# Optimization experiments

Hardware: AMD Instinct MI355X
Metric: run time of the kernel (lower is better)

## Reference

```python
import jax, jax.numpy as jnp
import numpy as np

BATCH = 64
INPUT_LENGTH = 128
N_TERMINALS = 64
N_NONTERMINALS = 128


def setup_inputs() -> dict:
    key = jax.random.key(0)
    k1, k2, k3 = jax.random.split(key, 3)
    input_tensor = jax.random.uniform(k1, (BATCH, INPUT_LENGTH, N_TERMINALS), dtype=jnp.float32)
    terminal_productions = jax.random.normal(k2, (N_NONTERMINALS, N_TERMINALS), dtype=jnp.float32)
    nonterminal_productions = jax.random.normal(k3, (N_NONTERMINALS, N_NONTERMINALS, N_TERMINALS), dtype=jnp.float32)
    return {
        "input_tensor": input_tensor,
        "terminal_productions": terminal_productions,
        "nonterminal_productions": nonterminal_productions,
    }


def reference(input_tensor, terminal_productions, nonterminal_productions):
    # input_tensor: [B, L, T]
    tp = jax.nn.sigmoid(terminal_productions)            # [N, T]
    ntp = jax.nn.sigmoid(nonterminal_productions)        # [N, N, T]

    # step 0: terminal production choices
    tpc = jnp.einsum('nt,bt->bn', tp, input_tensor[:, 0])  # [B, N]
    out0 = tpc[:, 0]                                        # [B]

    def step(carry, x_i):
        prev_choices, prev_out = carry                     # [B, N], [B]
        # per-batch nonterminal production choice matrix: [B, N, N]
        npc = jnp.clip(jnp.einsum('nmt,bt->bnm', ntp, x_i), 0.0, 1.0)
        cur = jnp.clip(jnp.einsum('bnm,bm->bn', npc, prev_choices), 0.0, 1.0)
        mask = x_i[:, N_TERMINALS - 1]                     # [B]
        out = prev_out * mask + cur[:, 0] * (1.0 - mask)
        return (cur, out), None

    xs = jnp.swapaxes(input_tensor[:, 1:], 0, 1)           # [L-1, B, T]
    (final_choices, final_out), _ = jax.lax.scan(step, (tpc, out0), xs)
    return final_out[:, None]                              # [B, 1]
```

## Files before the change

kernel.cpp:

```cpp
#include <hip/hip_runtime.h>
#include <hip/hip_bf16.h>

typedef unsigned int u32;
typedef unsigned char u8;
typedef _Float16 f16;
typedef f16 f16x2 __attribute__((ext_vector_type(2)));
typedef short s16x8 __attribute__((ext_vector_type(8)));
typedef float f32x4 __attribute__((ext_vector_type(4)));

#define BB 64
#define LL 128
#define TT 64
#define NN 128
#define NM (NN*NN)

__device__ __forceinline__ float sigf(float v) {
    return 1.0f / (1.0f + __expf(-v));
}

__device__ __forceinline__ float clip01(float v) {
    return fminf(fmaxf(v, 0.f), 1.f);
}

__device__ __forceinline__ u32 f2bf(float f) {
    u32 u = __builtin_bit_cast(u32, f);
    return (u + 0x7fffu + ((u >> 16) & 1u)) >> 16;
}

__device__ __forceinline__ float fdot2f(f16x2 wa, f16x2 xa, float ca) {
#if defined(__HIP_DEVICE_COMPILE__) && __has_builtin(__builtin_amdgcn_fdot2)
    return __builtin_amdgcn_fdot2(wa, xa, ca, false);
#else
    return ca + (float)wa[0] * (float)xa[0] + (float)wa[1] * (float)xa[1];
#endif
}

__device__ __forceinline__ u32 ud4(u32 a, u32 b, u32 c) {
#if defined(__HIP_DEVICE_COMPILE__) && __has_builtin(__builtin_amdgcn_udot4)
    return __builtin_amdgcn_udot4(a, b, c, false);
#else
    return c + (a & 255u) * (b & 255u) + ((a >> 8) & 255u) * ((b >> 8) & 255u)
             + ((a >> 16) & 255u) * ((b >> 16) & 255u) + (a >> 24) * (b >> 24);
#endif
}

__global__ __launch_bounds__(256) void pack_w(const float* __restrict__ ntp,
                                              ushort* __restrict__ wpk) {
    const int g = blockIdx.x * 256 + threadIdx.x;
    const int l = g & 63, h = (g >> 6) & 1, i = g >> 7;
    const int row = i * 16 + (l & 15);
    const int t0 = h * 32 + ((l >> 4) << 3);
    const float* src = ntp + row * 64 + t0;
    float4 f0 = *reinterpret_cast<const float4*>(src);
    float4 f1 = *reinterpret_cast<const float4*>(src + 4);
    float v[8] = {f0.x, f0.y, f0.z, f0.w, f1.x, f1.y, f1.z, f1.w};
    u32 o[4];
    #pragma unroll
    for (int q = 0; q < 4; ++q)
        o[q] = f2bf(sigf(v[2 * q])) | (f2bf(sigf(v[2 * q + 1])) << 16);
    uint4 ov; ov.x = o[0]; ov.y = o[1]; ov.z = o[2]; ov.w = o[3];
    *reinterpret_cast<uint4*>(wpk + (size_t)g * 8) = ov;
}

__global__ __launch_bounds__(256) void pack_x(const float* __restrict__ x_all,
                                              ushort* __restrict__ xpk) {
    const int g = blockIdx.x * 256 + threadIdx.x;
    const int l = g & 63, h = (g >> 6) & 1, j = (g >> 7) & 7, b = g >> 10;
    const int s = j * 16 + (l & 15);
    const int t0 = h * 32 + ((l >> 4) << 3);
    const float* src = x_all + ((size_t)b * LL + s) * TT + t0;
    float4 f0 = *reinterpret_cast<const float4*>(src);
    float4 f1 = *reinterpret_cast<const float4*>(src + 4);
    float v[8] = {f0.x, f0.y, f0.z, f0.w, f1.x, f1.y, f1.z, f1.w};
    u32 o[4];
    #pragma unroll
    for (int q = 0; q < 4; ++q)
        o[q] = f2bf(v[2 * q]) | (f2bf(v[2 * q + 1]) << 16);
    uint4 ov; ov.x = o[0]; ov.y = o[1]; ov.z = o[2]; ov.w = o[3];
    *reinterpret_cast<uint4*>(xpk + (size_t)g * 8) = ov;
}

__global__ __launch_bounds__(256) void gemm_mfma(const ushort* __restrict__ wpk,
                                                 const ushort* __restrict__ xpk,
                                                 u8* __restrict__ npc) {
    __shared__ __align__(16) u8 stg[4][16384];
    const int b = blockIdx.x >> 4;
    const int nb = blockIdx.x & 15;
    const int wv = threadIdx.x >> 6, l = threadIdx.x & 63;

    uint4 xf[8][2];
    #pragma unroll
    for (int j = 0; j < 8; ++j)
        #pragma unroll
        for (int h = 0; h < 2; ++h)
            xf[j][h] = *reinterpret_cast<const uint4*>(
                xpk + (size_t)(((b * 8 + j) * 2 + h) * 64 + l) * 8);

    const int c = l & 15, r0 = (l >> 4) * 4;
    u8* stw = stg[wv];
    const int khi  = (nb >> 3) * 8;
    const int nlow = (nb & 7) * 8;

    for (int mg2 = 0; mg2 < 2; ++mg2) {
        const int mg = wv * 2 + mg2;
        #pragma unroll
        for (int n_l = 0; n_l < 8; ++n_l) {
            const int i = (nb * 8 + n_l) * 8 + mg;
            uint4 a0 = *reinterpret_cast<const uint4*>(wpk + (size_t)((i * 2 + 0) * 64 + l) * 8);
            uint4 a1 = *reinterpret_cast<const uint4*>(wpk + (size_t)((i * 2 + 1) * 64 + l) * 8);
            const f32x4 z = {0.f, 0.f, 0.f, 0.f};
            f32x4 acc[8];
            #pragma unroll
            for (int j = 0; j < 8; ++j)
                acc[j] = __builtin_amdgcn_mfma_f32_16x16x32_bf16(
                    __builtin_bit_cast(s16x8, a0), __builtin_bit_cast(s16x8, xf[j][0]), z, 0, 0, 0);
            #pragma unroll
            for (int j = 0; j < 8; ++j)
                acc[j] = __builtin_amdgcn_mfma_f32_16x16x32_bf16(
                    __builtin_bit_cast(s16x8, a1), __builtin_bit_cast(s16x8, xf[j][1]), acc[j], 0, 0, 0);

            const int sk = (((n_l + c) & 7) << 4) + r0;
            #pragma unroll
            for (int j = 0; j < 8; ++j) {
                u32 w = 0;
                #pragma unroll
                for (int r = 0; r < 4; ++r) {
                    float q = clip01(acc[j][r]) * 255.f + 0.5f;
                    w |= ((u32)q) << (8 * r);
                }
                *reinterpret_cast<u32*>(stw + j * 2048 + c * 128 + sk) = w;
            }
        }
        asm volatile("s_waitcnt lgkmcnt(0)" ::: "memory");
        __builtin_amdgcn_sched_barrier(0);

        const int nr = l & 7;
        #pragma unroll
        for (int j = 0; j < 8; ++j) {
            #pragma unroll
            for (int half = 0; half < 2; ++half) {
                const int cc = half * 8 + (l >> 3);
                uint4 v = *reinterpret_cast<const uint4*>(
                    stw + j * 2048 + cc * 128 + (((nr + cc) & 7) << 4));
                *reinterpret_cast<uint4*>(npc + ((size_t)b << 21) + ((size_t)j << 18)
                    + ((size_t)cc << 14) + ((size_t)(mg + khi) << 10)
                    + ((nlow + nr) << 4)) = v;
            }
        }
        asm volatile("s_waitcnt lgkmcnt(0)" ::: "memory");
        __builtin_amdgcn_sched_barrier(0);
    }
}

__global__ __launch_bounds__(64) void recur4(const float* __restrict__ x_all,
                                             const float* __restrict__ tp,
                                             const u8* __restrict__ npc,
                                             float* __restrict__ outp) {
    __shared__ __align__(16) u8 prev_lds[2][128];
    __shared__ float masks_lds[128];
    __shared__ float tpc_lds[128];
    __shared__ float x0_lds[64];

    const int b = blockIdx.x, l = threadIdx.x;
    const u8* npcl = npc + ((size_t)b << 21) + ((size_t)l << 4);

    x0_lds[l] = x_all[(size_t)b * 8192 + l];
    masks_lds[l]      = x_all[(size_t)b * 8192 + l * 64 + 63];
    masks_lds[64 + l] = x_all[(size_t)b * 8192 + (64 + l) * 64 + 63];
    asm volatile("s_waitcnt lgkmcnt(0)" ::: "memory");
    __builtin_amdgcn_sched_barrier(0);

#define LOADSET(R, T) do { \
        int _t = (T) <= 127 ? (T) : 127; \
        const u8* _p = npcl + ((size_t)(_t >> 4) << 18) + ((size_t)(_t & 15) << 14); \
        _Pragma("unroll") \
        for (int _k = 0; _k < 16; ++_k) \
            R[_k] = *reinterpret_cast<const uint4*>(_p + _k * 1024); \
    } while (0)

    uint4 nA[16], nB[16];
    LOADSET(nA, 1);

    float a0 = 0.f, a1 = 0.f;
    #pragma unroll
    for (int t4 = 0; t4 < 16; ++t4) {
        float4 xv = *reinterpret_cast<const float4*>(x0_lds + t4 * 4);
        float4 w0 = *reinterpret_cast<const float4*>(tp + l * 64 + t4 * 4);
        float4 w1 = *reinterpret_cast<const float4*>(tp + (64 + l) * 64 + t4 * 4);
        a0 += sigf(w0.x) * xv.x; a0 += sigf(w0.y) * xv.y;
        a0 += sigf(w0.z) * xv.z; a0 += sigf(w0.w) * xv.w;
        a1 += sigf(w1.x) * xv.x; a1 += sigf(w1.y) * xv.y;
        a1 += sigf(w1.z) * xv.z; a1 += sigf(w1.w) * xv.w;
    }
    tpc_lds[l] = a0; tpc_lds[64 + l] = a1;
    float out_r = a0;
    asm volatile("s_waitcnt lgkmcnt(0)" ::: "memory");
    __builtin_amdgcn_sched_barrier(0);

    {
        float s0f = 0.f, s1f = 0.f;
        #pragma unroll
        for (int k = 0; k < 8; ++k) {
            u32 ax[4] = {nA[k].x, nA[k].y, nA[k].z, nA[k].w};
            u32 bx[4] = {nA[k + 8].x, nA[k + 8].y, nA[k + 8].z, nA[k + 8].w};
            #pragma unroll
            for (int w = 0; w < 4; ++w) {
                float4 tv = *reinterpret_cast<const float4*>(tpc_lds + k * 16 + w * 4);
                u32 aw = ax[w], bw = bx[w];
                s0f += (float)(aw & 255u) * tv.x + (float)((aw >> 8) & 255u) * tv.y
                     + (float)((aw >> 16) & 255u) * tv.z + (float)(aw >> 24) * tv.w;
                s1f += (float)(bw & 255u) * tv.x + (float)((bw >> 8) & 255u) * tv.y
                     + (float)((bw >> 16) & 255u) * tv.z + (float)(bw >> 24) * tv.w;
            }
        }
        float c0 = clip01(s0f * (1.f / 255.f));
        float c1 = clip01(s1f * (1.f / 255.f));
        float mk = masks_lds[1];
        if (l == 0) out_r = out_r * mk + c0 * (1.f - mk);
        prev_lds[0][l]      = (u8)(c0 * 255.f + 0.5f);
        prev_lds[0][64 + l] = (u8)(c1 * 255.f + 0.5f);
        asm volatile("s_waitcnt lgkmcnt(0)" ::: "memory");
        __builtin_amdgcn_sched_barrier(0);
    }

    int p = 0;
    LOADSET(nA, 2); LOADSET(nB, 3);

#define STEP(R, S) do { \
        uint4 pv[8]; \
        _Pragma("unroll") \
        for (int _q = 0; _q < 8; ++_q) \
            pv[_q] = *reinterpret_cast<const uint4*>(&prev_lds[p][_q * 16]); \
        float mk = masks_lds[(S)]; \
        u32 s0 = 0, t0 = 0, s1 = 0, t1 = 0; \
        _Pragma("unroll") \
        for (int _k = 0; _k < 4; ++_k) { \
            s0 = ud4(R[_k].x, pv[_k].x, s0); s0 = ud4(R[_k].y, pv[_k].y, s0); \
            s0 = ud4(R[_k].z, pv[_k].z, s0); s0 = ud4(R[_k].w, pv[_k].w, s0); \
        } \
        _Pragma("unroll") \
        for (int _k = 4; _k < 8; ++_k) { \
            t0 = ud4(R[_k].x, pv[_k].x, t0); t0 = ud4(R[_k].y, pv[_k].y, t0); \
            t0 = ud4(R[_k].z, pv[_k].z, t0); t0 = ud4(R[_k].w, pv[_k].w, t0); \
        } \
        _Pragma("unroll") \
        for (int _k = 8; _k < 12; ++_k) { \
            s1 = ud4(R[_k].x, pv[_k - 8].x, s1); s1 = ud4(R[_k].y, pv[_k - 8].y, s1); \
            s1 = ud4(R[_k].z, pv[_k - 8].z, s1); s1 = ud4(R[_k].w, pv[_k - 8].w, s1); \
        } \
        _Pragma("unroll") \
        for (int _k = 12; _k < 16; ++_k) { \
            t1 = ud4(R[_k].x, pv[_k - 8].x, t1); t1 = ud4(R[_k].y, pv[_k - 8].y, t1); \
            t1 = ud4(R[_k].z, pv[_k - 8].z, t1); t1 = ud4(R[_k].w, pv[_k - 8].w, t1); \
        } \
        float c0 = fminf((float)(s0 + t0) * (1.f / 65025.f), 1.f); \
        float c1 = fminf((float)(s1 + t1) * (1.f / 65025.f), 1.f); \
        u32 q0 = (u32)(c0 * 255.f + 0.5f), q1 = (u32)(c1 * 255.f + 0.5f); \
        if (l == 0) out_r = out_r * mk + c0 * (1.f - mk); \
        prev_lds[p ^ 1][l]      = (u8)q0; \
        prev_lds[p ^ 1][64 + l] = (u8)q1; \
        asm volatile("s_waitcnt lgkmcnt(0)" ::: "memory"); \
        __builtin_amdgcn_sched_barrier(0); \
        p ^= 1; \
    } while (0)

    for (int g = 0; g < 63; ++g) {
        const int s = 2 + 2 * g;
        STEP(nA, s);     LOADSET(nA, s + 2);
        STEP(nB, s + 1); LOADSET(nB, s + 3);
    }
#undef STEP
#undef LOADSET

    if (l == 0) outp[b] = out_r;
}

__global__ __launch_bounds__(256) void sig_transpose(const float* __restrict__ ntp,
                                                     u32* __restrict__ out) {
    __shared__ float lds[64 * 65];
    const int nm0 = blockIdx.x * 64;
    const int tid = threadIdx.x;
    #pragma unroll
    for (int it = 0; it < 16; ++it) {
        int idx = it * 256 + tid;
        int r = idx >> 6, c = idx & 63;
        lds[r * 65 + c] = sigf(ntp[(nm0 + r) * 64 + c]);
    }
    __syncthreads();
    #pragma unroll
    for (int it = 0; it < 8; ++it) {
        int o = it * 256 + tid;
        int tpi = o >> 6, r = o & 63;
        f16x2 h;
        h[0] = (f16)lds[r * 65 + 2 * tpi];
        h[1] = (f16)lds[r * 65 + 2 * tpi + 1];
        out[tpi * NM + nm0 + r] = __builtin_bit_cast(u32, h);
    }
}

__global__ __launch_bounds__(1024) void grammar_fused(
    const float* __restrict__ x_all,
    const float* __restrict__ tp,
    const u32*  __restrict__ ntpT2,
    float* __restrict__ outp) {
    __shared__ float x_lds[LL * TT];
    __shared__ float prevbuf[2][NN];
    __shared__ u32 x2_lds[2][32];

    const int b = blockIdx.x;
    const int tid = threadIdx.x;
    const int lane16 = tid & 15;
    const int g = tid >> 4;
    const int mbase = lane16 * 8;

    const float* xb = x_all + b * (LL * TT);
    #pragma unroll
    for (int it = 0; it < 8; ++it) {
        int idx = it * 1024 + tid;
        x_lds[idx] = xb[idx];
    }
    __syncthreads();

    if (tid < NN) {
        float acc = 0.f;
        #pragma unroll 8
        for (int t = 0; t < TT; ++t)
            acc += sigf(tp[tid * TT + t]) * x_lds[t];
        prevbuf[0][tid] = acc;
    }
    __syncthreads();
    float out_r = 0.f;
    if (tid == 0) out_r = prevbuf[0][0];

    int p = 0;
    for (int i0 = 1; i0 < LL; i0 += 2) {
        const int ns = (LL - i0) >= 2 ? 2 : 1;
        if (tid < 64) {
            int s = tid >> 5, tpi = tid & 31;
            f16x2 h;
            if (s < ns) {
                h[0] = (f16)x_lds[(i0 + s) * TT + 2 * tpi];
                h[1] = (f16)x_lds[(i0 + s) * TT + 2 * tpi + 1];
            } else {
                h[0] = (f16)0.f; h[1] = (f16)0.f;
            }
            x2_lds[s][tpi] = __builtin_bit_cast(u32, h);
        }
        __syncthreads();

        float acc[2][2][8];
        #pragma unroll
        for (int k = 0; k < 2; ++k)
            #pragma unroll
            for (int s = 0; s < 2; ++s)
                #pragma unroll
                for (int j = 0; j < 8; ++j) acc[k][s][j] = 0.f;

        #pragma unroll 2
        for (int tpi = 0; tpi < 32; ++tpi) {
            f16x2 xv0 = __builtin_bit_cast(f16x2, x2_lds[0][tpi]);
            f16x2 xv1 = __builtin_bit_cast(f16x2, x2_lds[1][tpi]);
            const u32* base = ntpT2 + tpi * NM + 8 * tid;
            #pragma unroll
            for (int k = 0; k < 2; ++k) {
                uint4 w0 = *reinterpret_cast<const uint4*>(base + 8192 * k);
                uint4 w1 = *reinterpret_cast<const uint4*>(base + 8192 * k + 4);
                u32 wv[8] = {w0.x, w0.y, w0.z, w0.w, w1.x, w1.y, w1.z, w1.w};
                #pragma unroll
                for (int j = 0; j < 8; ++j) {
                    f16x2 w = __builtin_bit_cast(f16x2, wv[j]);
                    acc[k][0][j] = fdot2f(w, xv0, acc[k][0][j]);
                    acc[k][1][j] = fdot2f(w, xv1, acc[k][1][j]);
                }
            }
        }

        for (int s = 0; s < ns; ++s) {
            float4 pv0 = *reinterpret_cast<const float4*>(&prevbuf[p][mbase]);
            float4 pv1 = *reinterpret_cast<const float4*>(&prevbuf[p][mbase + 4]);
            float pvv[8] = {pv0.x, pv0.y, pv0.z, pv0.w, pv1.x, pv1.y, pv1.z, pv1.w};
            #pragma unroll
            for (int k = 0; k < 2; ++k) {
                float part = 0.f;
                #pragma unroll
                for (int j = 0; j < 8; ++j) {
                    float npcv = clip01(acc[k][s][j]);
                    part += npcv * pvv[j];
                }
                part += __shfl_xor(part, 1);
                part += __shfl_xor(part, 2);
                part += __shfl_xor(part, 4);
                part += __shfl_xor(part, 8);
                if (lane16 == 0) {
                    float c = clip01(part);
                    prevbuf[p ^ 1][g + 64 * k] = c;
                    if (tid == 0 && k == 0) {
                        float mask = x_lds[(i0 + s) * TT + 63];
                        out_r = out_r * mask + c * (1.f - mask);
                    }
                }
            }
            p ^= 1;
            __syncthreads();
        }
    }

    if (tid == 0) outp[b] = out_r;
}

extern "C" void kernel_launch(void* const* d_in, const int* in_sizes, int n_in,
                              void* d_out, int out_size, void* d_ws, size_t ws_size,
                              hipStream_t stream) {
    const float* input_tensor = (const float*)d_in[0];
    const float* term_prod    = (const float*)d_in[1];
    const float* nonterm_prod = (const float*)d_in[2];
    float* outp = (float*)d_out;

    const size_t MB = 1024 * 1024;
    const size_t NPC_BYTES = 128 * MB;
    const size_t WPK_BYTES = 2 * MB;
    const size_t XPK_BYTES = 1 * MB;

    if (ws_size >= NPC_BYTES + WPK_BYTES + XPK_BYTES + MB) {
        u8* npcbuf  = (u8*)d_ws;
        ushort* wpk = (ushort*)((char*)d_ws + NPC_BYTES);
        ushort* xpk = (ushort*)((char*)d_ws + NPC_BYTES + WPK_BYTES);
        pack_w<<<512, 256, 0, stream>>>(nonterm_prod, wpk);
        pack_x<<<256, 256, 0, stream>>>(input_tensor, xpk);
        gemm_mfma<<<1024, 256, 0, stream>>>(wpk, xpk, npcbuf);
        recur4<<<BB, 64, 0, stream>>>(input_tensor, term_prod, npcbuf, outp);
    } else {
        u32* ntpT2 = (u32*)d_ws;
        sig_transpose<<<256, 256, 0, stream>>>(nonterm_prod, ntpT2);
        grammar_fused<<<BB, 1024, 0, stream>>>(input_tensor, term_prod, ntpT2, outp);
    }
}
```

Before: 93.59 us.

## Stream per-step npc tiles into LDS via async global_load_lds triple buffering

The recurrence kernel used to prefetch each step's 16 KB npc slice into registers with double buffering. It now issues direct global-to-LDS loads into a three-slot LDS ring, so each slice is requested three steps ahead, and waits on it with vmcnt counters. This frees the 32 prefetch registers and deepens the prefetch, adding an LDS read per step and relying on the vmcnt accounting of the LDS-bound loads being correct.

```diff
diff --git a/kernel.cpp b/kernel.cpp
--- a/kernel.cpp
+++ b/kernel.cpp
@@ -41,6 +41,16 @@
 #else
     return c + (a & 255u) * (b & 255u) + ((a >> 8) & 255u) * ((b >> 8) & 255u)
              + ((a >> 16) & 255u) * ((b >> 16) & 255u) + (a >> 24) * (b >> 24);
+#endif
+}
+
+__device__ __forceinline__ void gload_lds16(const u8* g, u8* lds) {
+#if defined(__HIP_DEVICE_COMPILE__)
+    __builtin_amdgcn_global_load_lds(
+        (const __attribute__((address_space(1))) u32*)g,
+        (__attribute__((address_space(3))) u32*)lds, 16, 0, 0);
+#else
+    (void)g; (void)lds;
 #endif
 }
 
@@ -152,34 +162,24 @@
     }
 }
 
-__global__ __launch_bounds__(64) void recur4(const float* __restrict__ x_all,
-                                             const float* __restrict__ tp,
-                                             const u8* __restrict__ npc,
-                                             float* __restrict__ outp) {
+__global__ __launch_bounds__(64, 1) void recur7(const float* __restrict__ x_all,
+                                                const float* __restrict__ tp,
+                                                const u8* __restrict__ npc,
+                                                float* __restrict__ outp) {
+    __shared__ __align__(16) u8 npc_lds[3 * 16384];
     __shared__ __align__(16) u8 prev_lds[2][128];
     __shared__ float masks_lds[128];
     __shared__ float tpc_lds[128];
     __shared__ float x0_lds[64];
 
     const int b = blockIdx.x, l = threadIdx.x;
-    const u8* npcl = npc + ((size_t)b << 21) + ((size_t)l << 4);
+    const u8* npcg = npc + ((size_t)b << 21);
 
     x0_lds[l] = x_all[(size_t)b * 8192 + l];
     masks_lds[l]      = x_all[(size_t)b * 8192 + l * 64 + 63];
     masks_lds[64 + l] = x_all[(size_t)b * 8192 + (64 + l) * 64 + 63];
     asm volatile("s_waitcnt lgkmcnt(0)" ::: "memory");
     __builtin_amdgcn_sched_barrier(0);
-
-#define LOADSET(R, T) do { \
-        int _t = (T) <= 127 ? (T) : 127; \
-        const u8* _p = npcl + ((size_t)(_t >> 4) << 18) + ((size_t)(_t & 15) << 14); \
-        _Pragma("unroll") \
-        for (int _k = 0; _k < 16; ++_k) \
-            R[_k] = *reinterpret_cast<const uint4*>(_p + _k * 1024); \
-    } while (0)
-
-    uint4 nA[16], nB[16];
-    LOADSET(nA, 1);
 
     float a0 = 0.f, a1 = 0.f;
     #pragma unroll
@@ -194,15 +194,33 @@
     }
     tpc_lds[l] = a0; tpc_lds[64 + l] = a1;
     float out_r = a0;
-    asm volatile("s_waitcnt lgkmcnt(0)" ::: "memory");
+    asm volatile("s_waitcnt vmcnt(0) lgkmcnt(0)" ::: "memory");
     __builtin_amdgcn_sched_barrier(0);
 
+#define STAGE(SLOT_OFF, T) do { \
+        int _t = (T) <= 127 ? (T) : 127; \
+        const u8* _src = npcg + ((size_t)(_t >> 4) << 18) \
+                              + ((size_t)(_t & 15) << 14) + ((u32)l << 4); \
+        _Pragma("unroll") \
+        for (int _k = 0; _k < 16; ++_k) \
+            gload_lds16(_src + _k * 1024, &npc_lds[(SLOT_OFF) + _k * 1024]); \
+        __builtin_amdgcn_sched_barrier(0); \
+    } while (0)
+
+    STAGE(0, 1); STAGE(16384, 2); STAGE(32768, 3);
+
     {
+        asm volatile("s_waitcnt vmcnt(32)" ::: "memory");
+        __builtin_amdgcn_sched_barrier(0);
+        uint4 nk[16];
+        #pragma unroll
+        for (int k = 0; k < 16; ++k)
+            nk[k] = *reinterpret_cast<const uint4*>(&npc_lds[k * 1024 + l * 16]);
         float s0f = 0.f, s1f = 0.f;
         #pragma unroll
         for (int k = 0; k < 8; ++k) {
-            u32 ax[4] = {nA[k].x, nA[k].y, nA[k].z, nA[k].w};
-            u32 bx[4] = {nA[k + 8].x, nA[k + 8].y, nA[k + 8].z, nA[k + 8].w};
+            u32 ax[4] = {nk[k].x, nk[k].y, nk[k].z, nk[k].w};
+            u32 bx[4] = {nk[k + 8].x, nk[k + 8].y, nk[k + 8].z, nk[k + 8].w};
             #pragma unroll
             for (int w = 0; w < 4; ++w) {
                 float4 tv = *reinterpret_cast<const float4*>(tpc_lds + k * 16 + w * 4);
@@ -222,11 +240,17 @@
         asm volatile("s_waitcnt lgkmcnt(0)" ::: "memory");
         __builtin_amdgcn_sched_barrier(0);
     }
+    STAGE(0, 4);
 
     int p = 0;
-    LOADSET(nA, 2); LOADSET(nB, 3);
-
-#define STEP(R, S) do { \
+
+#define STEP(SLOT_OFF, S) do { \
+        asm volatile("s_waitcnt vmcnt(32)" ::: "memory"); \
+        __builtin_amdgcn_sched_barrier(0); \
+        uint4 nk[16]; \
+        _Pragma("unroll") \
+        for (int _k = 0; _k < 16; ++_k) \
+            nk[_k] = *reinterpret_cast<const uint4*>(&npc_lds[(SLOT_OFF) + _k * 1024 + l * 16]); \
         uint4 pv[8]; \
         _Pragma("unroll") \
         for (int _q = 0; _q < 8; ++_q) \
@@ -235,23 +259,23 @@
         u32 s0 = 0, t0 = 0, s1 = 0, t1 = 0; \
         _Pragma("unroll") \
         for (int _k = 0; _k < 4; ++_k) { \
-            s0 = ud4(R[_k].x, pv[_k].x, s0); s0 = ud4(R[_k].y, pv[_k].y, s0); \
-            s0 = ud4(R[_k].z, pv[_k].z, s0); s0 = ud4(R[_k].w, pv[_k].w, s0); \
+            s0 = ud4(nk[_k].x, pv[_k].x, s0); s0 = ud4(nk[_k].y, pv[_k].y, s0); \
+            s0 = ud4(nk[_k].z, pv[_k].z, s0); s0 = ud4(nk[_k].w, pv[_k].w, s0); \
         } \
         _Pragma("unroll") \
         for (int _k = 4; _k < 8; ++_k) { \
-            t0 = ud4(R[_k].x, pv[_k].x, t0); t0 = ud4(R[_k].y, pv[_k].y, t0); \
-            t0 = ud4(R[_k].z, pv[_k].z, t0); t0 = ud4(R[_k].w, pv[_k].w, t0); \
+            t0 = ud4(nk[_k].x, pv[_k].x, t0); t0 = ud4(nk[_k].y, pv[_k].y, t0); \
+            t0 = ud4(nk[_k].z, pv[_k].z, t0); t0 = ud4(nk[_k].w, pv[_k].w, t0); \
         } \
         _Pragma("unroll") \
         for (int _k = 8; _k < 12; ++_k) { \
-            s1 = ud4(R[_k].x, pv[_k - 8].x, s1); s1 = ud4(R[_k].y, pv[_k - 8].y, s1); \
-            s1 = ud4(R[_k].z, pv[_k - 8].z, s1); s1 = ud4(R[_k].w, pv[_k - 8].w, s1); \
+            s1 = ud4(nk[_k].x, pv[_k - 8].x, s1); s1 = ud4(nk[_k].y, pv[_k - 8].y, s1); \
+            s1 = ud4(nk[_k].z, pv[_k - 8].z, s1); s1 = ud4(nk[_k].w, pv[_k - 8].w, s1); \
         } \
         _Pragma("unroll") \
         for (int _k = 12; _k < 16; ++_k) { \
-            t1 = ud4(R[_k].x, pv[_k - 8].x, t1); t1 = ud4(R[_k].y, pv[_k - 8].y, t1); \
-            t1 = ud4(R[_k].z, pv[_k - 8].z, t1); t1 = ud4(R[_k].w, pv[_k - 8].w, t1); \
+            t1 = ud4(nk[_k].x, pv[_k - 8].x, t1); t1 = ud4(nk[_k].y, pv[_k - 8].y, t1); \
+            t1 = ud4(nk[_k].z, pv[_k - 8].z, t1); t1 = ud4(nk[_k].w, pv[_k - 8].w, t1); \
         } \
         float c0 = fminf((float)(s0 + t0) * (1.f / 65025.f), 1.f); \
         float c1 = fminf((float)(s1 + t1) * (1.f / 65025.f), 1.f); \
@@ -264,13 +288,20 @@
         p ^= 1; \
     } while (0)
 
-    for (int g = 0; g < 63; ++g) {
-        const int s = 2 + 2 * g;
-        STEP(nA, s);     LOADSET(nA, s + 2);
-        STEP(nB, s + 1); LOADSET(nB, s + 3);
-    }
+    for (int g = 0; g < 41; ++g) {
+        const int s = 2 + 3 * g;
+        STEP(16384, s);     STAGE(16384, s + 3);
+        STEP(32768, s + 1); STAGE(32768, s + 4);
+        STEP(0,     s + 2); STAGE(0,     s + 5);
+    }
+    STEP(16384, 125); STAGE(16384, 127);
+    STEP(32768, 126); STAGE(32768, 127);
+    STEP(0,     127); STAGE(0,     127);
+    asm volatile("s_waitcnt vmcnt(0)" ::: "memory");
+    __builtin_amdgcn_sched_barrier(0);
+
 #undef STEP
-#undef LOADSET
+#undef STAGE
 
     if (l == 0) outp[b] = out_r;
 }
@@ -428,7 +459,7 @@
         pack_w<<<512, 256, 0, stream>>>(nonterm_prod, wpk);
         pack_x<<<256, 256, 0, stream>>>(input_tensor, xpk);
         gemm_mfma<<<1024, 256, 0, stream>>>(wpk, xpk, npcbuf);
-        recur4<<<BB, 64, 0, stream>>>(input_tensor, term_prod, npcbuf, outp);
+        recur7<<<BB, 64, 0, stream>>>(input_tensor, term_prod, npcbuf, outp);
     } else {
         u32* ntpT2 = (u32*)d_ws;
         sig_transpose<<<256, 256, 0, stream>>>(nonterm_prod, ntpT2);
```

Result: slower. 121.2 us (+29.5%).
